# Optimization experiments

Hardware: AMD Instinct MI355X
Metric: run time of the kernel (lower is better)

The kernel has to match this reference:

```python
import jax, jax.numpy as jnp
import numpy as np

B, S, H, NH, NKV, D = 1, 2048, 4096, 32, 8, 128
ROPE_BASE = 1000000.0


def setup_inputs() -> dict:
    key = jax.random.key(0)
    k0, k1, k2, k3, k4 = jax.random.split(key, 5)
    hidden_states = jax.random.normal(k0, (B, S, H), dtype=jnp.float32)
    Wq = jax.random.normal(k1, (NH * D, H), dtype=jnp.float32) * 0.02
    Wk = jax.random.normal(k2, (NKV * D, H), dtype=jnp.float32) * 0.02
    Wv = jax.random.normal(k3, (NKV * D, H), dtype=jnp.float32) * 0.02
    Wo = jax.random.normal(k4, (NH * D, NH * D), dtype=jnp.float32) * 0.02
    # RoPE tables (Mistral rope_theta = 1e6), concatenated-halves layout
    inv_freq = 1.0 / (ROPE_BASE ** (jnp.arange(0, D, 2, dtype=jnp.float32) / D))
    pos = jnp.arange(S, dtype=jnp.float32)
    freqs = pos[:, None] * inv_freq[None, :]            # [S, D/2]
    emb = jnp.concatenate([freqs, freqs], axis=-1)       # [S, D]
    cos = jnp.cos(emb)[None]                             # [1, S, D]
    sin = jnp.sin(emb)[None]
    # additive causal mask [1,1,S,S]
    causal = jnp.tril(jnp.ones((S, S), dtype=bool))
    attention_mask = jnp.where(causal, 0.0, -1e9).astype(jnp.float32)[None, None]
    return {"hidden_states": hidden_states, "cos": cos, "sin": sin,
            "attention_mask": attention_mask, "Wq": Wq, "Wk": Wk, "Wv": Wv, "Wo": Wo}


def _rotate_half(x):
    d = x.shape[-1] // 2
    return jnp.concatenate([-x[..., d:], x[..., :d]], axis=-1)


def reference(hidden_states, cos, sin, attention_mask, Wq, Wk, Wv, Wo):
    b, s, _ = hidden_states.shape
    nh = Wq.shape[0] // D
    nkv = Wk.shape[0] // D
    g = nh // nkv  # GQA groups
    scaling = D ** -0.5

    q = (hidden_states @ Wq.T).reshape(b, s, nh, D).transpose(0, 2, 1, 3)   # [b,nh,s,d]
    k = (hidden_states @ Wk.T).reshape(b, s, nkv, D).transpose(0, 2, 1, 3)  # [b,nkv,s,d]
    v = (hidden_states @ Wv.T).reshape(b, s, nkv, D).transpose(0, 2, 1, 3)

    c = cos[:, None]  # [b,1,s,d] broadcast over heads (unsqueeze_dim=1)
    sn = sin[:, None]
    q = q * c + _rotate_half(q) * sn
    k = k * c + _rotate_half(k) * sn

    # grouped-query attention without materializing repeated K/V
    qg = q.reshape(b, nkv, g, s, D)
    attn = jnp.einsum('bkgqd,bksd->bkgqs', qg, k) * scaling
    attn = attn + attention_mask[:, :, None]  # broadcast [1,1,1,s,s]
    w = jax.nn.softmax(attn.astype(jnp.float32), axis=-1).astype(q.dtype)
    out = jnp.einsum('bkgqs,bksd->bkgqd', w, v)  # [b,nkv,g,s,d]
    out = out.reshape(b, nh, s, D).transpose(0, 2, 1, 3).reshape(b, s, nh * D)
    return out @ Wo.T
```

## Files before the change

kernel.cpp:

```cpp
#include <hip/hip_runtime.h>
#include <hip/hip_bf16.h>
#include <cstdint>
#include <cstddef>

#define S_LEN 2048
#define HID   4096
#define NHEAD 32
#define NKVH  8
#define HD    128
#define QKV_STR 6144

typedef __bf16 bf16x8 __attribute__((ext_vector_type(8)));
typedef float  f32x4  __attribute__((ext_vector_type(4)));
typedef float  f32x16 __attribute__((ext_vector_type(16)));
typedef unsigned uint32x2_t __attribute__((ext_vector_type(2)));

__device__ __forceinline__ unsigned short f2bf(float f) {
  union { float f; unsigned int u; } c; c.f = f;
  unsigned int u = c.u;
  return (unsigned short)((u + 0x7fffu + ((u >> 16) & 1u)) >> 16);
}
__device__ __forceinline__ float bf2f(unsigned short b) {
  union { unsigned int u; float f; } c; c.u = ((unsigned int)b) << 16;
  return c.f;
}
__device__ __forceinline__ void gload16(const void* g, void* l) {
  __builtin_amdgcn_global_load_lds((const __attribute__((address_space(1))) void*)g,
                                   (__attribute__((address_space(3))) void*)l, 16, 0, 0);
}

__global__ void cvt_multi(const float* __restrict__ s0, const float* __restrict__ s1,
                          const float* __restrict__ s2, const float* __restrict__ s3,
                          const float* __restrict__ s4,
                          unsigned short* __restrict__ d0, unsigned short* __restrict__ d1,
                          unsigned short* __restrict__ d2, unsigned short* __restrict__ d3,
                          unsigned short* __restrict__ d4,
                          int n0, int n1, int n2, int n3, int n4c) {
  const float* src; unsigned short* dst; int n;
  switch (blockIdx.y) {
    case 0: src = s0; dst = d0; n = n0; break;
    case 1: src = s1; dst = d1; n = n1; break;
    case 2: src = s2; dst = d2; n = n2; break;
    case 3: src = s3; dst = d3; n = n3; break;
    default: src = s4; dst = d4; n = n4c; break;
  }
  int i = blockIdx.x * blockDim.x + threadIdx.x;
  int stride = gridDim.x * blockDim.x;
  for (; i < n; i += stride) {
    float4 v = ((const float4*)src)[i];
    ushort4 o;
    o.x = f2bf(v.x); o.y = f2bf(v.y); o.z = f2bf(v.z); o.w = f2bf(v.w);
    ((ushort4*)dst)[i] = o;
  }
}

template <bool F32OUT>
__global__ __launch_bounds__(256)
void gemm_bt(const unsigned short* __restrict__ A,
             const unsigned short* __restrict__ Bm,
             void* __restrict__ Cout, int N, int K) {
  __shared__ __align__(16) unsigned short lA[3][128 * 32];
  __shared__ __align__(16) unsigned short lB[3][128 * 32];
  const int tid = threadIdx.x;
  const int lane = tid & 63, wid = tid >> 6;
  const int l15 = lane & 15, lg = lane >> 4;
  const int wr = (wid >> 1) * 64, wc = (wid & 1) * 64;
  const int nwg = gridDim.x * 16;
  int bid = blockIdx.x + blockIdx.y * gridDim.x;
  bid = (bid & 7) * (nwg >> 3) + (bid >> 3);
  const int bm = bid & 15, bn = bid >> 4;

  f32x4 acc[4][4] = {};
  const unsigned short* Ab = A + (size_t)bm * 128 * K;
  const unsigned short* Bb = Bm + (size_t)bn * 128 * K;

  auto stage = [&](int t, int buf) {
    const int k0 = t * 32;
#pragma unroll
    for (int i = 0; i < 2; ++i) {
      int c = tid + i * 256;
      int row = c >> 2, sl = c & 3;
      int g = sl ^ ((row >> 1) & 3);
      gload16(Ab + (size_t)row * K + k0 + g * 8, (char*)lA[buf] + c * 16);
      gload16(Bb + (size_t)row * K + k0 + g * 8, (char*)lB[buf] + c * 16);
    }
  };

  const int nt = K / 32;
  stage(0, 0);
  if (nt > 1) stage(1, 1);
  const int swz = (l15 >> 1) & 3;

  int cur = 0;
  for (int t = 0; t < nt; ++t) {
    if (t + 1 < nt) asm volatile("s_waitcnt vmcnt(4)" ::: "memory");
    else            asm volatile("s_waitcnt vmcnt(0)" ::: "memory");
    __builtin_amdgcn_s_barrier();
    __builtin_amdgcn_sched_barrier(0);
    if (t + 2 < nt) { int nb = cur + 2; if (nb >= 3) nb -= 3; stage(t + 2, nb); }
    bf16x8 af[4], bfr[4];
#pragma unroll
    for (int m = 0; m < 4; ++m)
      af[m] = *(const bf16x8*)&lA[cur][(wr + m * 16 + l15) * 32 + ((lg ^ swz) * 8)];
#pragma unroll
    for (int n = 0; n < 4; ++n)
      bfr[n] = *(const bf16x8*)&lB[cur][(wc + n * 16 + l15) * 32 + ((lg ^ swz) * 8)];
#pragma unroll
    for (int m = 0; m < 4; ++m)
#pragma unroll
      for (int n = 0; n < 4; ++n)
        acc[m][n] = __builtin_amdgcn_mfma_f32_16x16x32_bf16(af[m], bfr[n], acc[m][n], 0, 0, 0);
    ++cur; if (cur >= 3) cur -= 3;
  }
  const int r0 = bm * 128 + wr + 4 * lg;
  const int c0 = bn * 128 + wc + l15;
#pragma unroll
  for (int m = 0; m < 4; ++m)
#pragma unroll
    for (int n = 0; n < 4; ++n)
#pragma unroll
      for (int j = 0; j < 4; ++j) {
        size_t idx = (size_t)(r0 + m * 16 + j) * N + (c0 + n * 16);
        if (F32OUT) ((float*)Cout)[idx] = acc[m][n][j];
        else        ((unsigned short*)Cout)[idx] = f2bf(acc[m][n][j]);
      }
}

__global__ void rope_kernel(unsigned short* __restrict__ X,
                            const float* __restrict__ cp,
                            const float* __restrict__ sp, int lognh, int rs) {
  int idx = blockIdx.x * blockDim.x + threadIdx.x;
  int d = idx & 63;
  int head = (idx >> 6) & ((1 << lognh) - 1);
  int s = idx >> (6 + lognh);
  float c = cp[s * 128 + d], sn = sp[s * 128 + d];
  size_t base = (size_t)s * rs + (head << 7) + d;
  float x1 = bf2f(X[base]);
  float x2 = bf2f(X[base + 64]);
  X[base]      = f2bf(x1 * c - x2 * sn);
  X[base + 64] = f2bf(x2 * c + x1 * sn);
}

__global__ __launch_bounds__(256)
void transpose_v(const unsigned short* __restrict__ qkv,
                 unsigned short* __restrict__ VT) {
  __shared__ __align__(16) unsigned short tile[128 * 128];
  const int tid = threadIdx.x;
  const int s0 = blockIdx.x * 128;
  const int kvh = blockIdx.y;
  const unsigned short* src = qkv + 5120 + kvh * 128;
#pragma unroll
  for (int i = 0; i < 8; ++i) {
    int c = tid + i * 256;
    int s = c >> 4, dc = c & 15;
    int f = (s ^ (s >> 3)) & 7;
    uint4 v = *(const uint4*)(src + (size_t)(s0 + s) * QKV_STR + dc * 8);
    *(uint4*)&tile[s * 128 + ((dc ^ f) * 8)] = v;
  }
  __syncthreads();
#pragma unroll
  for (int i = 0; i < 8; ++i) {
    int c = tid + i * 256;
    int d = c >> 4, sc = c & 15;
    unsigned short tmp[8];
#pragma unroll
    for (int j = 0; j < 8; ++j) {
      int s = sc * 8 + j;
      int f = (s ^ (s >> 3)) & 7;
      tmp[j] = tile[s * 128 + (((d >> 3) ^ f) * 8) + (d & 7)];
    }
    *(uint4*)(VT + ((size_t)kvh * 128 + d) * S_LEN + s0 + sc * 8) = *(uint4*)tmp;
  }
}

#define CROW(r) (((r) & 3) + 8 * ((r) >> 2) + 4 * hi)
__global__ __launch_bounds__(256, 2)
void flash_attn(const unsigned short* __restrict__ qkv,
                const unsigned short* __restrict__ VT,
                const float* __restrict__ cp,
                const float* __restrict__ sp,
                unsigned short* __restrict__ Og) {
  __shared__ __align__(16) unsigned short lK[2 * 64 * 128];
  __shared__ __align__(16) unsigned short lVt[2 * 128 * 64];
  const int tid = threadIdx.x;
  const int lane = tid & 63, w = tid >> 6;
  const int l31 = lane & 31, hi = lane >> 5;
  const int h = blockIdx.y, kvh = h >> 2;
  const int qt = (h & 16) ? blockIdx.x : (15 - blockIdx.x);
  const int nt = 2 * qt + 2;
  const int qlane = qt * 128 + w * 32 + l31;
  const int qmaxw = qt * 128 + w * 32 + 31;
  const float S2 = 0.12752960f;

  bf16x8 qf[8];
  {
    const unsigned short* qp = qkv + (size_t)qlane * QKV_STR + h * HD + hi * 8;
#pragma unroll
    for (int ks = 0; ks < 8; ++ks) qf[ks] = *(const bf16x8*)(qp + ks * 16);
    const float* crow = cp + (size_t)qlane * 128 + hi * 8;
    const float* srow = sp + (size_t)qlane * 128 + hi * 8;
#pragma unroll
    for (int ks = 0; ks < 4; ++ks) {
      float4 c0 = *(const float4*)(crow + ks * 16);
      float4 c1 = *(const float4*)(crow + ks * 16 + 4);
      float4 s0 = *(const float4*)(srow + ks * 16);
      float4 s1 = *(const float4*)(srow + ks * 16 + 4);
      float cc[8] = {c0.x, c0.y, c0.z, c0.w, c1.x, c1.y, c1.z, c1.w};
      float ss[8] = {s0.x, s0.y, s0.z, s0.w, s1.x, s1.y, s1.z, s1.w};
#pragma unroll
      for (int j = 0; j < 8; ++j) {
        float x1 = (float)qf[ks][j], x2 = (float)qf[ks + 4][j];
        qf[ks][j]     = (__bf16)(x1 * cc[j] - x2 * ss[j]);
        qf[ks + 4][j] = (__bf16)(x2 * cc[j] + x1 * ss[j]);
      }
    }
  }
  f32x16 accO[4] = {};
  float m_run = -3e38f, l_run = 0.f;

  const unsigned short* Kb0 = qkv + 4096 + kvh * HD;
  const unsigned short* VTh = VT + (size_t)kvh * 128 * S_LEN;

  auto stageK = [&](int t, int buf) {
    const unsigned short* Kb = Kb0 + (size_t)(t * 64) * QKV_STR;
    char* dst = (char*)(lK + buf * (64 * 128));
#pragma unroll
    for (int i = 0; i < 4; ++i) {
      int c = tid + i * 256;
      int row = c >> 4, s = c & 15;
      gload16(Kb + (size_t)row * QKV_STR + ((s ^ (row & 7)) * 8), dst + c * 16);
    }
  };
  auto stageV = [&](int t, int buf) {
    const unsigned short* Vb = VTh + t * 64;
    char* dst = (char*)(lVt + buf * (128 * 64));
#pragma unroll
    for (int i = 0; i < 4; ++i) {
      int c = tid + i * 256;
      int d = c >> 3, s = c & 7;
      gload16(Vb + (size_t)d * S_LEN + ((s ^ (d & 7)) * 8), dst + c * 16);
    }
  };

  stageK(0, 0);
  stageV(0, 0);
  __syncthreads();

  int cur = 0;
  for (int t = 0; t < nt; ++t) {
    const bool pf = (t + 1 < nt);
    if (pf) { stageK(t + 1, cur ^ 1); stageV(t + 1, cur ^ 1); }

#pragma unroll
    for (int c2 = 0; c2 < 2; ++c2) {
      const int kvb = t * 64 + c2 * 32;
      if (kvb > qmaxw) continue;
      f32x16 st = {};
      const unsigned short* lKc = lK + cur * (64 * 128) + c2 * 32 * 128;
      __builtin_amdgcn_s_setprio(1);
#pragma unroll
      for (int ks = 0; ks < 8; ++ks) {
        bf16x8 kf = *(const bf16x8*)&lKc[l31 * 128 + (((ks * 2 + hi) ^ (l31 & 7)) * 8)];
        st = __builtin_amdgcn_mfma_f32_32x32x16_bf16(kf, qf[ks], st, 0, 0, 0);
      }
      __builtin_amdgcn_s_setprio(0);
      if (kvb + 31 > qt * 128 + w * 32) {
#pragma unroll
        for (int r = 0; r < 16; ++r)
          if (kvb + CROW(r) > qlane) st[r] = -3e38f;
      }
      float t0 = fmaxf(st[0], st[1]),  t1 = fmaxf(st[2], st[3]);
      float t2 = fmaxf(st[4], st[5]),  t3 = fmaxf(st[6], st[7]);
      float t4 = fmaxf(st[8], st[9]),  t5 = fmaxf(st[10], st[11]);
      float t6 = fmaxf(st[12], st[13]), t7 = fmaxf(st[14], st[15]);
      float tm = fmaxf(fmaxf(fmaxf(t0, t1), fmaxf(t2, t3)),
                       fmaxf(fmaxf(t4, t5), fmaxf(t6, t7)));
      tm = fmaxf(tm, __shfl_xor(tm, 32));
      const bool skip = __all((tm - m_run) * S2 <= 8.0f);
      float corr = 1.f;
      if (!skip) {
        float mnew = fmaxf(m_run, tm);
        corr = __builtin_amdgcn_exp2f((m_run - mnew) * S2);
        m_run = mnew;
      }
      const float mS2 = m_run * S2;
      float p[16];
#pragma unroll
      for (int r = 0; r < 16; ++r) p[r] = __builtin_amdgcn_exp2f(st[r] * S2 - mS2);
      float s0b = (p[0] + p[1]) + (p[2] + p[3]);
      float s1b = (p[4] + p[5]) + (p[6] + p[7]);
      float s2b = (p[8] + p[9]) + (p[10] + p[11]);
      float s3b = (p[12] + p[13]) + (p[14] + p[15]);
      float rsum = (s0b + s1b) + (s2b + s3b);
      rsum += __shfl_xor(rsum, 32);
      l_run = l_run * corr + rsum;
      if (!skip) {
#pragma unroll
        for (int db = 0; db < 4; ++db) accO[db] = accO[db] * corr;
      }
      unsigned wpk[8];
#pragma unroll
      for (int i = 0; i < 8; ++i) {
        __hip_bfloat162 b2 = __float22bfloat162_rn(float2{p[2 * i], p[2 * i + 1]});
        wpk[i] = *(unsigned*)&b2;
      }
      int4 pa0i, pa1i;
#if __has_builtin(__builtin_amdgcn_permlane32_swap)
      uint32x2_t r0 = __builtin_amdgcn_permlane32_swap(wpk[0], wpk[2], false, false);
      uint32x2_t r1 = __builtin_amdgcn_permlane32_swap(wpk[1], wpk[3], false, false);
      uint32x2_t r2 = __builtin_amdgcn_permlane32_swap(wpk[4], wpk[6], false, false);
      uint32x2_t r3 = __builtin_amdgcn_permlane32_swap(wpk[5], wpk[7], false, false);
      pa0i.x = (int)r0.x; pa0i.y = (int)r1.x; pa0i.z = (int)r0.y; pa0i.w = (int)r1.y;
      pa1i.x = (int)r2.x; pa1i.y = (int)r3.x; pa1i.z = (int)r2.y; pa1i.w = (int)r3.y;
#else
      unsigned xpk[8];
#pragma unroll
      for (int i = 0; i < 8; ++i) xpk[i] = (unsigned)__shfl_xor((int)wpk[i], 32);
      pa0i.x = hi ? (int)xpk[2] : (int)wpk[0]; pa0i.y = hi ? (int)xpk[3] : (int)wpk[1];
      pa0i.z = hi ? (int)wpk[2] : (int)xpk[0]; pa0i.w = hi ? (int)wpk[3] : (int)xpk[1];
      pa1i.x = hi ? (int)xpk[6] : (int)wpk[4]; pa1i.y = hi ? (int)xpk[7] : (int)wpk[5];
      pa1i.z = hi ? (int)wpk[6] : (int)xpk[4]; pa1i.w = hi ? (int)wpk[7] : (int)xpk[5];
#endif
      bf16x8 pa0 = *(bf16x8*)&pa0i, pa1 = *(bf16x8*)&pa1i;
      const unsigned short* lVc = lVt + cur * (128 * 64);
      __builtin_amdgcn_s_setprio(1);
#pragma unroll
      for (int db = 0; db < 4; ++db) {
        int d = db * 32 + l31;
#pragma unroll
        for (int ks2 = 0; ks2 < 2; ++ks2) {
          int ck = c2 * 4 + ks2 * 2 + hi;
          bf16x8 vf = *(const bf16x8*)&lVc[d * 64 + ((ck ^ (d & 7)) * 8)];
          accO[db] = __builtin_amdgcn_mfma_f32_32x32x16_bf16(vf, ks2 ? pa1 : pa0, accO[db], 0, 0, 0);
        }
      }
      __builtin_amdgcn_s_setprio(0);
    }
    __syncthreads();
    cur ^= 1;
  }

  const float invl = 1.0f / l_run;
  unsigned short* orow = Og + (size_t)(qt * 128 + w * 32 + l31) * HID + h * HD;
#pragma unroll
  for (int db = 0; db < 4; ++db)
#pragma unroll
    for (int rr = 0; rr < 4; ++rr) {
      int d0 = db * 32 + rr * 8 + 4 * hi;
      ushort4 o;
      o.x = f2bf(accO[db][rr * 4 + 0] * invl);
      o.y = f2bf(accO[db][rr * 4 + 1] * invl);
      o.z = f2bf(accO[db][rr * 4 + 2] * invl);
      o.w = f2bf(accO[db][rr * 4 + 3] * invl);
      *(ushort4*)(orow + d0) = o;
    }
}

extern "C" void kernel_launch(void* const* d_in, const int* in_sizes, int n_in,
                              void* d_out, int out_size, void* d_ws, size_t ws_size,
                              hipStream_t stream) {
  const float* hs   = (const float*)d_in[0];
  const float* cosp = (const float*)d_in[1];
  const float* sinp = (const float*)d_in[2];
  const float* Wq = (const float*)d_in[4];
  const float* Wk = (const float*)d_in[5];
  const float* Wv = (const float*)d_in[6];
  const float* Wo = (const float*)d_in[7];
  float* out = (float*)d_out;

  uint8_t* ws = (uint8_t*)d_ws;
  size_t off = 0;
  auto alloc = [&](size_t bytes) { void* p = ws + off; off += bytes; return p; };
  unsigned short* hidB  = (unsigned short*)alloc((size_t)S_LEN * HID * 2);
  unsigned short* wqkvB = (unsigned short*)alloc((size_t)QKV_STR * HID * 2);
  unsigned short* woB   = (unsigned short*)alloc((size_t)HID * HID * 2);
  unsigned short* qkvB  = (unsigned short*)alloc((size_t)S_LEN * QKV_STR * 2);
  unsigned short* aoB   = (unsigned short*)alloc((size_t)S_LEN * HID * 2);
  unsigned short* vtB   = (unsigned short*)alloc((size_t)NKVH * HD * S_LEN * 2);

  cvt_multi<<<dim3(1024, 5), 256, 0, stream>>>(
      hs, Wq, Wk, Wv, Wo,
      hidB, wqkvB, wqkvB + (size_t)HID * HID, wqkvB + (size_t)(HID + 1024) * HID, woB,
      S_LEN * HID / 4, HID * HID / 4, 1024 * HID / 4, 1024 * HID / 4, HID * HID / 4);

  gemm_bt<false><<<dim3(QKV_STR / 128, S_LEN / 128), 256, 0, stream>>>(
      hidB, wqkvB, qkvB, QKV_STR, HID);

  rope_kernel<<<(S_LEN * NKVH * 64) / 256, 256, 0, stream>>>(qkvB + HID, cosp, sinp, 3, QKV_STR);

  transpose_v<<<dim3(S_LEN / 128, NKVH), 256, 0, stream>>>(qkvB, vtB);

  flash_attn<<<dim3(S_LEN / 128, NHEAD), 256, 0, stream>>>(qkvB, vtB, cosp, sinp, aoB);

  gemm_bt<true><<<dim3(HID / 128, S_LEN / 128), 256, 0, stream>>>(
      aoB, woB, out, HID, HID);
}
```

Baseline: 334.6 us.

## Fuse K RoPE into V transpose and process 64-key tiles with one softmax

The separate RoPE kernel for K is merged into the V-transpose kernel, which removes one launch and gives each block one (seq tile, kv head) slice to rotate. In the flash-attention loop, the two 32-key sub-chunks of each 64-key tile are now handled together. Both QK^T MFMA chains are issued first, then a single max/exp/rescale pass covers all 64 keys. This halves the per-chunk max, shuffle, __all vote and accumulator-rescale overhead, at the cost of more live registers under launch bounds of 2 blocks per unit.

```diff
diff --git a/kernel.cpp b/kernel.cpp
--- a/kernel.cpp
+++ b/kernel.cpp
@@ -126,28 +126,27 @@
       }
 }
 
-__global__ void rope_kernel(unsigned short* __restrict__ X,
-                            const float* __restrict__ cp,
-                            const float* __restrict__ sp, int lognh, int rs) {
-  int idx = blockIdx.x * blockDim.x + threadIdx.x;
-  int d = idx & 63;
-  int head = (idx >> 6) & ((1 << lognh) - 1);
-  int s = idx >> (6 + lognh);
-  float c = cp[s * 128 + d], sn = sp[s * 128 + d];
-  size_t base = (size_t)s * rs + (head << 7) + d;
-  float x1 = bf2f(X[base]);
-  float x2 = bf2f(X[base + 64]);
-  X[base]      = f2bf(x1 * c - x2 * sn);
-  X[base + 64] = f2bf(x2 * c + x1 * sn);
-}
-
 __global__ __launch_bounds__(256)
-void transpose_v(const unsigned short* __restrict__ qkv,
-                 unsigned short* __restrict__ VT) {
+void rope_transpose(unsigned short* __restrict__ qkv,
+                    const float* __restrict__ cp,
+                    const float* __restrict__ sp,
+                    unsigned short* __restrict__ VT) {
   __shared__ __align__(16) unsigned short tile[128 * 128];
   const int tid = threadIdx.x;
   const int s0 = blockIdx.x * 128;
   const int kvh = blockIdx.y;
+  unsigned short* K = qkv + 4096 + kvh * 128;
+#pragma unroll 4
+  for (int i = 0; i < 32; ++i) {
+    int idx = tid + i * 256;
+    int sl = idx >> 6, d = idx & 63;
+    float c = cp[(size_t)(s0 + sl) * 128 + d];
+    float sn = sp[(size_t)(s0 + sl) * 128 + d];
+    size_t base = (size_t)(s0 + sl) * QKV_STR + d;
+    float x1 = bf2f(K[base]), x2 = bf2f(K[base + 64]);
+    K[base]      = f2bf(x1 * c - x2 * sn);
+    K[base + 64] = f2bf(x2 * c + x1 * sn);
+  }
   const unsigned short* src = qkv + 5120 + kvh * 128;
 #pragma unroll
   for (int i = 0; i < 8; ++i) {
@@ -174,6 +173,7 @@
 }
 
 #define CROW(r) (((r) & 3) + 8 * ((r) >> 2) + 4 * hi)
+#define MAX3(a, b, c) fmaxf(fmaxf(a, b), c)
 __global__ __launch_bounds__(256, 2)
 void flash_attn(const unsigned short* __restrict__ qkv,
                 const unsigned short* __restrict__ VT,
@@ -188,8 +188,9 @@
   const int h = blockIdx.y, kvh = h >> 2;
   const int qt = (h & 16) ? blockIdx.x : (15 - blockIdx.x);
   const int nt = 2 * qt + 2;
-  const int qlane = qt * 128 + w * 32 + l31;
-  const int qmaxw = qt * 128 + w * 32 + 31;
+  const int qminw = qt * 128 + w * 32;
+  const int qlane = qminw + l31;
+  const int qmaxw = qminw + 31;
   const float S2 = 0.12752960f;
 
   bf16x8 qf[8];
@@ -251,30 +252,57 @@
     const bool pf = (t + 1 < nt);
     if (pf) { stageK(t + 1, cur ^ 1); stageV(t + 1, cur ^ 1); }
 
-#pragma unroll
-    for (int c2 = 0; c2 < 2; ++c2) {
-      const int kvb = t * 64 + c2 * 32;
-      if (kvb > qmaxw) continue;
-      f32x16 st = {};
-      const unsigned short* lKc = lK + cur * (64 * 128) + c2 * 32 * 128;
+    const int kvb0 = t * 64, kvb1 = kvb0 + 32;
+    if (kvb0 <= qmaxw) {
+      const bool live1 = (kvb1 <= qmaxw);
+      const unsigned short* lKc = lK + cur * (64 * 128);
+      f32x16 st0 = {}, st1 = {};
       __builtin_amdgcn_s_setprio(1);
 #pragma unroll
       for (int ks = 0; ks < 8; ++ks) {
         bf16x8 kf = *(const bf16x8*)&lKc[l31 * 128 + (((ks * 2 + hi) ^ (l31 & 7)) * 8)];
-        st = __builtin_amdgcn_mfma_f32_32x32x16_bf16(kf, qf[ks], st, 0, 0, 0);
+        st0 = __builtin_amdgcn_mfma_f32_32x32x16_bf16(kf, qf[ks], st0, 0, 0, 0);
+      }
+      if (live1) {
+        const unsigned short* lKc1 = lKc + 32 * 128;
+#pragma unroll
+        for (int ks = 0; ks < 8; ++ks) {
+          bf16x8 kf = *(const bf16x8*)&lKc1[l31 * 128 + (((ks * 2 + hi) ^ (l31 & 7)) * 8)];
+          st1 = __builtin_amdgcn_mfma_f32_32x32x16_bf16(kf, qf[ks], st1, 0, 0, 0);
+        }
       }
       __builtin_amdgcn_s_setprio(0);
-      if (kvb + 31 > qt * 128 + w * 32) {
+      if (kvb0 + 31 > qminw) {
 #pragma unroll
         for (int r = 0; r < 16; ++r)
-          if (kvb + CROW(r) > qlane) st[r] = -3e38f;
-      }
-      float t0 = fmaxf(st[0], st[1]),  t1 = fmaxf(st[2], st[3]);
-      float t2 = fmaxf(st[4], st[5]),  t3 = fmaxf(st[6], st[7]);
-      float t4 = fmaxf(st[8], st[9]),  t5 = fmaxf(st[10], st[11]);
-      float t6 = fmaxf(st[12], st[13]), t7 = fmaxf(st[14], st[15]);
-      float tm = fmaxf(fmaxf(fmaxf(t0, t1), fmaxf(t2, t3)),
-                       fmaxf(fmaxf(t4, t5), fmaxf(t6, t7)));
+          if (kvb0 + CROW(r) > qlane) st0[r] = -3e38f;
+      }
+      if (live1) {
+        if (kvb1 + 31 > qminw) {
+#pragma unroll
+          for (int r = 0; r < 16; ++r)
+            if (kvb1 + CROW(r) > qlane) st1[r] = -3e38f;
+        }
+      } else {
+#pragma unroll
+        for (int r = 0; r < 16; ++r) st1[r] = -3e38f;
+      }
+      float u0 = MAX3(st0[0], st0[1], st0[2]);
+      float u1 = MAX3(st0[3], st0[4], st0[5]);
+      float u2 = MAX3(st0[6], st0[7], st0[8]);
+      float u3 = MAX3(st0[9], st0[10], st0[11]);
+      float u4 = MAX3(st0[12], st0[13], st0[14]);
+      float u5 = MAX3(st0[15], st1[0], st1[1]);
+      float u6 = MAX3(st1[2], st1[3], st1[4]);
+      float u7 = MAX3(st1[5], st1[6], st1[7]);
+      float u8 = MAX3(st1[8], st1[9], st1[10]);
+      float u9 = MAX3(st1[11], st1[12], st1[13]);
+      float uA = fmaxf(st1[14], st1[15]);
+      float v0 = MAX3(u0, u1, u2);
+      float v1 = MAX3(u3, u4, u5);
+      float v2 = MAX3(u6, u7, u8);
+      float v3 = fmaxf(u9, uA);
+      float tm = fmaxf(fmaxf(v0, v1), fmaxf(v2, v3));
       tm = fmaxf(tm, __shfl_xor(tm, 32));
       const bool skip = __all((tm - m_run) * S2 <= 8.0f);
       float corr = 1.f;
@@ -284,54 +312,94 @@
         m_run = mnew;
       }
       const float mS2 = m_run * S2;
-      float p[16];
-#pragma unroll
-      for (int r = 0; r < 16; ++r) p[r] = __builtin_amdgcn_exp2f(st[r] * S2 - mS2);
-      float s0b = (p[0] + p[1]) + (p[2] + p[3]);
-      float s1b = (p[4] + p[5]) + (p[6] + p[7]);
-      float s2b = (p[8] + p[9]) + (p[10] + p[11]);
-      float s3b = (p[12] + p[13]) + (p[14] + p[15]);
-      float rsum = (s0b + s1b) + (s2b + s3b);
+#pragma unroll
+      for (int r = 0; r < 16; ++r) st0[r] = __builtin_amdgcn_exp2f(st0[r] * S2 - mS2);
+#pragma unroll
+      for (int r = 0; r < 16; ++r) st1[r] = __builtin_amdgcn_exp2f(st1[r] * S2 - mS2);
+      float a0 = (st0[0] + st0[1]) + (st0[2] + st0[3]);
+      float a1 = (st0[4] + st0[5]) + (st0[6] + st0[7]);
+      float a2 = (st0[8] + st0[9]) + (st0[10] + st0[11]);
+      float a3 = (st0[12] + st0[13]) + (st0[14] + st0[15]);
+      float a4 = (st1[0] + st1[1]) + (st1[2] + st1[3]);
+      float a5 = (st1[4] + st1[5]) + (st1[6] + st1[7]);
+      float a6 = (st1[8] + st1[9]) + (st1[10] + st1[11]);
+      float a7 = (st1[12] + st1[13]) + (st1[14] + st1[15]);
+      float rsum = ((a0 + a1) + (a2 + a3)) + ((a4 + a5) + (a6 + a7));
       rsum += __shfl_xor(rsum, 32);
       l_run = l_run * corr + rsum;
       if (!skip) {
 #pragma unroll
         for (int db = 0; db < 4; ++db) accO[db] = accO[db] * corr;
       }
-      unsigned wpk[8];
-#pragma unroll
-      for (int i = 0; i < 8; ++i) {
-        __hip_bfloat162 b2 = __float22bfloat162_rn(float2{p[2 * i], p[2 * i + 1]});
-        wpk[i] = *(unsigned*)&b2;
-      }
-      int4 pa0i, pa1i;
+      bf16x8 pa00, pa01, pa10 = {}, pa11 = {};
+      {
+        unsigned wpk[8];
+#pragma unroll
+        for (int i = 0; i < 8; ++i) {
+          __hip_bfloat162 b2 = __float22bfloat162_rn(float2{st0[2 * i], st0[2 * i + 1]});
+          wpk[i] = *(unsigned*)&b2;
+        }
+        int4 p0i, p1i;
 #if __has_builtin(__builtin_amdgcn_permlane32_swap)
-      uint32x2_t r0 = __builtin_amdgcn_permlane32_swap(wpk[0], wpk[2], false, false);
-      uint32x2_t r1 = __builtin_amdgcn_permlane32_swap(wpk[1], wpk[3], false, false);
-      uint32x2_t r2 = __builtin_amdgcn_permlane32_swap(wpk[4], wpk[6], false, false);
-      uint32x2_t r3 = __builtin_amdgcn_permlane32_swap(wpk[5], wpk[7], false, false);
-      pa0i.x = (int)r0.x; pa0i.y = (int)r1.x; pa0i.z = (int)r0.y; pa0i.w = (int)r1.y;
-      pa1i.x = (int)r2.x; pa1i.y = (int)r3.x; pa1i.z = (int)r2.y; pa1i.w = (int)r3.y;
+        uint32x2_t r0 = __builtin_amdgcn_permlane32_swap(wpk[0], wpk[2], false, false);
+        uint32x2_t r1 = __builtin_amdgcn_permlane32_swap(wpk[1], wpk[3], false, false);
+        uint32x2_t r2 = __builtin_amdgcn_permlane32_swap(wpk[4], wpk[6], false, false);
+        uint32x2_t r3 = __builtin_amdgcn_permlane32_swap(wpk[5], wpk[7], false, false);
+        p0i.x = (int)r0.x; p0i.y = (int)r1.x; p0i.z = (int)r0.y; p0i.w = (int)r1.y;
+        p1i.x = (int)r2.x; p1i.y = (int)r3.x; p1i.z = (int)r2.y; p1i.w = (int)r3.y;
 #else
-      unsigned xpk[8];
-#pragma unroll
-      for (int i = 0; i < 8; ++i) xpk[i] = (unsigned)__shfl_xor((int)wpk[i], 32);
-      pa0i.x = hi ? (int)xpk[2] : (int)wpk[0]; pa0i.y = hi ? (int)xpk[3] : (int)wpk[1];
-      pa0i.z = hi ? (int)wpk[2] : (int)xpk[0]; pa0i.w = hi ? (int)wpk[3] : (int)xpk[1];
-      pa1i.x = hi ? (int)xpk[6] : (int)wpk[4]; pa1i.y = hi ? (int)xpk[7] : (int)wpk[5];
-      pa1i.z = hi ? (int)wpk[6] : (int)xpk[4]; pa1i.w = hi ? (int)wpk[7] : (int)xpk[5];
+        unsigned xpk[8];
+#pragma unroll
+        for (int i = 0; i < 8; ++i) xpk[i] = (unsigned)__shfl_xor((int)wpk[i], 32);
+        p0i.x = hi ? (int)xpk[2] : (int)wpk[0]; p0i.y = hi ? (int)xpk[3] : (int)wpk[1];
+        p0i.z = hi ? (int)wpk[2] : (int)xpk[0]; p0i.w = hi ? (int)wpk[3] : (int)xpk[1];
+        p1i.x = hi ? (int)xpk[6] : (int)wpk[4]; p1i.y = hi ? (int)xpk[7] : (int)wpk[5];
+        p1i.z = hi ? (int)wpk[6] : (int)xpk[4]; p1i.w = hi ? (int)wpk[7] : (int)xpk[5];
 #endif
-      bf16x8 pa0 = *(bf16x8*)&pa0i, pa1 = *(bf16x8*)&pa1i;
+        pa00 = *(bf16x8*)&p0i; pa01 = *(bf16x8*)&p1i;
+      }
+      if (live1) {
+        unsigned wpk[8];
+#pragma unroll
+        for (int i = 0; i < 8; ++i) {
+          __hip_bfloat162 b2 = __float22bfloat162_rn(float2{st1[2 * i], st1[2 * i + 1]});
+          wpk[i] = *(unsigned*)&b2;
+        }
+        int4 p0i, p1i;
+#if __has_builtin(__builtin_amdgcn_permlane32_swap)
+        uint32x2_t r0 = __builtin_amdgcn_permlane32_swap(wpk[0], wpk[2], false, false);
+        uint32x2_t r1 = __builtin_amdgcn_permlane32_swap(wpk[1], wpk[3], false, false);
+        uint32x2_t r2 = __builtin_amdgcn_permlane32_swap(wpk[4], wpk[6], false, false);
+        uint32x2_t r3 = __builtin_amdgcn_permlane32_swap(wpk[5], wpk[7], false, false);
+        p0i.x = (int)r0.x; p0i.y = (int)r1.x; p0i.z = (int)r0.y; p0i.w = (int)r1.y;
+        p1i.x = (int)r2.x; p1i.y = (int)r3.x; p1i.z = (int)r2.y; p1i.w = (int)r3.y;
+#else
+        unsigned xpk[8];
+#pragma unroll
+        for (int i = 0; i < 8; ++i) xpk[i] = (unsigned)__shfl_xor((int)wpk[i], 32);
+        p0i.x = hi ? (int)xpk[2] : (int)wpk[0]; p0i.y = hi ? (int)xpk[3] : (int)wpk[1];
+        p0i.z = hi ? (int)wpk[2] : (int)xpk[0]; p0i.w = hi ? (int)wpk[3] : (int)xpk[1];
+        p1i.x = hi ? (int)xpk[6] : (int)wpk[4]; p1i.y = hi ? (int)xpk[7] : (int)wpk[5];
+        p1i.z = hi ? (int)wpk[6] : (int)xpk[4]; p1i.w = hi ? (int)wpk[7] : (int)xpk[5];
+#endif
+        pa10 = *(bf16x8*)&p0i; pa11 = *(bf16x8*)&p1i;
+      }
       const unsigned short* lVc = lVt + cur * (128 * 64);
       __builtin_amdgcn_s_setprio(1);
 #pragma unroll
       for (int db = 0; db < 4; ++db) {
         int d = db * 32 + l31;
-#pragma unroll
-        for (int ks2 = 0; ks2 < 2; ++ks2) {
-          int ck = c2 * 4 + ks2 * 2 + hi;
-          bf16x8 vf = *(const bf16x8*)&lVc[d * 64 + ((ck ^ (d & 7)) * 8)];
-          accO[db] = __builtin_amdgcn_mfma_f32_32x32x16_bf16(vf, ks2 ? pa1 : pa0, accO[db], 0, 0, 0);
+        int dsw = d & 7;
+        bf16x8 vf;
+        vf = *(const bf16x8*)&lVc[d * 64 + (((0 + hi) ^ dsw) * 8)];
+        accO[db] = __builtin_amdgcn_mfma_f32_32x32x16_bf16(vf, pa00, accO[db], 0, 0, 0);
+        vf = *(const bf16x8*)&lVc[d * 64 + (((2 + hi) ^ dsw) * 8)];
+        accO[db] = __builtin_amdgcn_mfma_f32_32x32x16_bf16(vf, pa01, accO[db], 0, 0, 0);
+        if (live1) {
+          vf = *(const bf16x8*)&lVc[d * 64 + (((4 + hi) ^ dsw) * 8)];
+          accO[db] = __builtin_amdgcn_mfma_f32_32x32x16_bf16(vf, pa10, accO[db], 0, 0, 0);
+          vf = *(const bf16x8*)&lVc[d * 64 + (((6 + hi) ^ dsw) * 8)];
+          accO[db] = __builtin_amdgcn_mfma_f32_32x32x16_bf16(vf, pa11, accO[db], 0, 0, 0);
         }
       }
       __builtin_amdgcn_s_setprio(0);
@@ -386,9 +454,7 @@
   gemm_bt<false><<<dim3(QKV_STR / 128, S_LEN / 128), 256, 0, stream>>>(
       hidB, wqkvB, qkvB, QKV_STR, HID);
 
-  rope_kernel<<<(S_LEN * NKVH * 64) / 256, 256, 0, stream>>>(qkvB + HID, cosp, sinp, 3, QKV_STR);
-
-  transpose_v<<<dim3(S_LEN / 128, NKVH), 256, 0, stream>>>(qkvB, vtB);
+  rope_transpose<<<dim3(S_LEN / 128, NKVH), 256, 0, stream>>>(qkvB, cosp, sinp, vtB);
 
   flash_attn<<<dim3(S_LEN / 128, NHEAD), 256, 0, stream>>>(qkvB, vtB, cosp, sinp, aoB);
 
```

After: 338.4 us. No clear change (+1.1%).

## Fuse K RoPE into V transpose and move Wo conversion into attention tail

Applied to the files above, without the earlier changes.

Merges the standalone K RoPE kernel into the V transpose kernel, so one launch handles both, tiled per 128-row block and KV head. It also drops the Wo fp32-to-bf16 conversion from the initial convert kernel and appends it to the end of the flash attention kernel, spread over all 512 attention blocks. The aim is fewer launches and hiding the Wo conversion traffic inside the unevenly loaded attention tail. The risks are extra memory traffic and register pressure in the attention kernel, and a small RoPE kernel with only 128 blocks of parallelism.

```diff
diff --git a/kernel.cpp b/kernel.cpp
--- a/kernel.cpp
+++ b/kernel.cpp
@@ -31,18 +31,15 @@
 
 __global__ void cvt_multi(const float* __restrict__ s0, const float* __restrict__ s1,
                           const float* __restrict__ s2, const float* __restrict__ s3,
-                          const float* __restrict__ s4,
                           unsigned short* __restrict__ d0, unsigned short* __restrict__ d1,
                           unsigned short* __restrict__ d2, unsigned short* __restrict__ d3,
-                          unsigned short* __restrict__ d4,
-                          int n0, int n1, int n2, int n3, int n4c) {
+                          int n0, int n1, int n2, int n3) {
   const float* src; unsigned short* dst; int n;
   switch (blockIdx.y) {
     case 0: src = s0; dst = d0; n = n0; break;
     case 1: src = s1; dst = d1; n = n1; break;
     case 2: src = s2; dst = d2; n = n2; break;
-    case 3: src = s3; dst = d3; n = n3; break;
-    default: src = s4; dst = d4; n = n4c; break;
+    default: src = s3; dst = d3; n = n3; break;
   }
   int i = blockIdx.x * blockDim.x + threadIdx.x;
   int stride = gridDim.x * blockDim.x;
@@ -126,28 +123,27 @@
       }
 }
 
-__global__ void rope_kernel(unsigned short* __restrict__ X,
-                            const float* __restrict__ cp,
-                            const float* __restrict__ sp, int lognh, int rs) {
-  int idx = blockIdx.x * blockDim.x + threadIdx.x;
-  int d = idx & 63;
-  int head = (idx >> 6) & ((1 << lognh) - 1);
-  int s = idx >> (6 + lognh);
-  float c = cp[s * 128 + d], sn = sp[s * 128 + d];
-  size_t base = (size_t)s * rs + (head << 7) + d;
-  float x1 = bf2f(X[base]);
-  float x2 = bf2f(X[base + 64]);
-  X[base]      = f2bf(x1 * c - x2 * sn);
-  X[base + 64] = f2bf(x2 * c + x1 * sn);
-}
-
 __global__ __launch_bounds__(256)
-void transpose_v(const unsigned short* __restrict__ qkv,
-                 unsigned short* __restrict__ VT) {
+void rope_transpose(unsigned short* __restrict__ qkv,
+                    const float* __restrict__ cp,
+                    const float* __restrict__ sp,
+                    unsigned short* __restrict__ VT) {
   __shared__ __align__(16) unsigned short tile[128 * 128];
   const int tid = threadIdx.x;
   const int s0 = blockIdx.x * 128;
   const int kvh = blockIdx.y;
+  unsigned short* K = qkv + 4096 + kvh * 128;
+#pragma unroll 4
+  for (int i = 0; i < 32; ++i) {
+    int idx = tid + i * 256;
+    int sl = idx >> 6, d = idx & 63;
+    float c = cp[(size_t)(s0 + sl) * 128 + d];
+    float sn = sp[(size_t)(s0 + sl) * 128 + d];
+    size_t base = (size_t)(s0 + sl) * QKV_STR + d;
+    float x1 = bf2f(K[base]), x2 = bf2f(K[base + 64]);
+    K[base]      = f2bf(x1 * c - x2 * sn);
+    K[base + 64] = f2bf(x2 * c + x1 * sn);
+  }
   const unsigned short* src = qkv + 5120 + kvh * 128;
 #pragma unroll
   for (int i = 0; i < 8; ++i) {
@@ -179,7 +175,9 @@
                 const unsigned short* __restrict__ VT,
                 const float* __restrict__ cp,
                 const float* __restrict__ sp,
-                unsigned short* __restrict__ Og) {
+                unsigned short* __restrict__ Og,
+                const float* __restrict__ Wo,
+                unsigned short* __restrict__ woB) {
   __shared__ __align__(16) unsigned short lK[2 * 64 * 128];
   __shared__ __align__(16) unsigned short lVt[2 * 128 * 64];
   const int tid = threadIdx.x;
@@ -188,8 +186,9 @@
   const int h = blockIdx.y, kvh = h >> 2;
   const int qt = (h & 16) ? blockIdx.x : (15 - blockIdx.x);
   const int nt = 2 * qt + 2;
-  const int qlane = qt * 128 + w * 32 + l31;
-  const int qmaxw = qt * 128 + w * 32 + 31;
+  const int qminw = qt * 128 + w * 32;
+  const int qlane = qminw + l31;
+  const int qmaxw = qminw + 31;
   const float S2 = 0.12752960f;
 
   bf16x8 qf[8];
@@ -264,7 +263,7 @@
         st = __builtin_amdgcn_mfma_f32_32x32x16_bf16(kf, qf[ks], st, 0, 0, 0);
       }
       __builtin_amdgcn_s_setprio(0);
-      if (kvb + 31 > qt * 128 + w * 32) {
+      if (kvb + 31 > qminw) {
 #pragma unroll
         for (int r = 0; r < 16; ++r)
           if (kvb + CROW(r) > qlane) st[r] = -3e38f;
@@ -354,6 +353,17 @@
       o.w = f2bf(accO[db][rr * 4 + 3] * invl);
       *(ushort4*)(orow + d0) = o;
     }
+
+  {
+    const int gb = blockIdx.y * gridDim.x + blockIdx.x;
+    const int total = HID * HID / 4;
+    for (int i = gb * 256 + tid; i < total; i += 512 * 256) {
+      float4 v = ((const float4*)Wo)[i];
+      ushort4 o;
+      o.x = f2bf(v.x); o.y = f2bf(v.y); o.z = f2bf(v.z); o.w = f2bf(v.w);
+      ((ushort4*)woB)[i] = o;
+    }
+  }
 }
 
 extern "C" void kernel_launch(void* const* d_in, const int* in_sizes, int n_in,
@@ -378,19 +388,18 @@
   unsigned short* aoB   = (unsigned short*)alloc((size_t)S_LEN * HID * 2);
   unsigned short* vtB   = (unsigned short*)alloc((size_t)NKVH * HD * S_LEN * 2);
 
-  cvt_multi<<<dim3(1024, 5), 256, 0, stream>>>(
-      hs, Wq, Wk, Wv, Wo,
-      hidB, wqkvB, wqkvB + (size_t)HID * HID, wqkvB + (size_t)(HID + 1024) * HID, woB,
-      S_LEN * HID / 4, HID * HID / 4, 1024 * HID / 4, 1024 * HID / 4, HID * HID / 4);
+  cvt_multi<<<dim3(1024, 4), 256, 0, stream>>>(
+      hs, Wq, Wk, Wv,
+      hidB, wqkvB, wqkvB + (size_t)HID * HID, wqkvB + (size_t)(HID + 1024) * HID,
+      S_LEN * HID / 4, HID * HID / 4, 1024 * HID / 4, 1024 * HID / 4);
 
   gemm_bt<false><<<dim3(QKV_STR / 128, S_LEN / 128), 256, 0, stream>>>(
       hidB, wqkvB, qkvB, QKV_STR, HID);
 
-  rope_kernel<<<(S_LEN * NKVH * 64) / 256, 256, 0, stream>>>(qkvB + HID, cosp, sinp, 3, QKV_STR);
-
-  transpose_v<<<dim3(S_LEN / 128, NKVH), 256, 0, stream>>>(qkvB, vtB);
-
-  flash_attn<<<dim3(S_LEN / 128, NHEAD), 256, 0, stream>>>(qkvB, vtB, cosp, sinp, aoB);
+  rope_transpose<<<dim3(S_LEN / 128, NKVH), 256, 0, stream>>>(qkvB, cosp, sinp, vtB);
+
+  flash_attn<<<dim3(S_LEN / 128, NHEAD), 256, 0, stream>>>(
+      qkvB, vtB, cosp, sinp, aoB, Wo, woB);
 
   gemm_bt<true><<<dim3(HID / 128, S_LEN / 128), 256, 0, stream>>>(
       aoB, woB, out, HID, HID);
```

Measured after the change: 335.7 us. About the same (+0.3%).
